# Performance work log

Hardware: AMD Instinct MI355X
Metric: run time of the kernel (lower is better)

Reference implementation:

```python
import jax, jax.numpy as jnp
import numpy as np

EPS = 1e-12  # matches torch F.normalize default eps

def setup_inputs() -> dict:
    key = jax.random.key(0)
    k1, k2 = jax.random.split(key)
    query = jax.random.normal(k1, (8, 2048, 512), dtype=jnp.float32)
    support = jax.random.normal(k2, (8, 4096, 512), dtype=jnp.float32)
    return {"query": query, "support": support}

def _l2_normalize(x):
    # torch.nn.functional.normalize(x, dim=-1): x / max(||x||, eps)
    n = jnp.sqrt(jnp.sum(x * x, axis=-1, keepdims=True))
    return x / jnp.maximum(n, EPS)

def reference(query, support):
    # cosine distance: 1 - q_hat @ s_hat^T  -> [B, Nq, Ns]
    qn = _l2_normalize(query)
    sn = _l2_normalize(support)
    dist = 1.0 - jnp.einsum('bqd,bsd->bqs', qn, sn)
    min_d = jnp.min(dist, axis=2)        # [B, Nq]
    return jnp.mean(min_d, axis=1)       # [B]
```

## Files before the change

### kernel.cpp

```cpp
#include <hip/hip_runtime.h>
#include <hip/hip_bf16.h>

typedef __attribute__((ext_vector_type(8))) short short8;
typedef __attribute__((ext_vector_type(4))) float f32x4;
typedef __attribute__((ext_vector_type(16))) float f32x16;
typedef __attribute__((ext_vector_type(8))) int int8v;

#define D   512
#define NQ  2048
#define NS  4096
#define NB  8
#define BM  128
#define BN  128
#define BK  32

typedef const __attribute__((address_space(1))) unsigned int gas_uint;
typedef __attribute__((address_space(3))) unsigned int las_uint;

__device__ __forceinline__ short f2bf(float f) {
  unsigned u = __builtin_bit_cast(unsigned, f);
  unsigned r = u + 0x7fffu + ((u >> 16) & 1u);
  return (short)(r >> 16);
}

__device__ __forceinline__ short8 pack8(float4 a, float4 b, float r) {
  short8 o;
  o[0] = f2bf(a.x * r); o[1] = f2bf(a.y * r); o[2] = f2bf(a.z * r); o[3] = f2bf(a.w * r);
  o[4] = f2bf(b.x * r); o[5] = f2bf(b.y * r); o[6] = f2bf(b.z * r); o[7] = f2bf(b.w * r);
  return o;
}

__global__ void normcvt8_kernel(const float* __restrict__ q, const float* __restrict__ s,
                                unsigned char* __restrict__ qn, unsigned char* __restrict__ sn,
                                unsigned* __restrict__ maxenc) {
  if (blockIdx.x < 64) maxenc[(blockIdx.x << 8) | threadIdx.x] = 0;
  int wave = blockIdx.x * 4 + (threadIdx.x >> 6);
  int lane = threadIdx.x & 63;
  const int NQR = NB * NQ;
  const float4* src; unsigned char* dst;
  if (wave < NQR) { src = (const float4*)(q + (size_t)wave * D); dst = qn + (size_t)wave * D; }
  else {
    size_t w = wave - NQR;
    src = (const float4*)(s + w * D); dst = sn + w * D;
  }
  float4 a = src[lane * 2];
  float4 b = src[lane * 2 + 1];
  float ss = a.x*a.x + a.y*a.y + a.z*a.z + a.w*a.w
           + b.x*b.x + b.y*b.y + b.z*b.z + b.w*b.w;
  #pragma unroll
  for (int m = 32; m >= 1; m >>= 1) ss += __shfl_xor(ss, m, 64);
  float r = 1.0f / fmaxf(sqrtf(ss), 1e-12f);
  int w0 = __builtin_amdgcn_cvt_pk_fp8_f32(a.x * r, a.y * r, 0, false);
  w0     = __builtin_amdgcn_cvt_pk_fp8_f32(a.z * r, a.w * r, w0, true);
  int w1 = __builtin_amdgcn_cvt_pk_fp8_f32(b.x * r, b.y * r, 0, false);
  w1     = __builtin_amdgcn_cvt_pk_fp8_f32(b.z * r, b.w * r, w1, true);
  *(int2*)(dst + lane * 8) = make_int2(w0, w1);
}

__global__ __launch_bounds__(512, 4) void cosmax5_kernel(
    const unsigned char* __restrict__ Qn, const unsigned char* __restrict__ Sn,
    unsigned int* __restrict__ maxenc)
{
  __shared__ __align__(16) unsigned char As[BM * 128];
  __shared__ __align__(16) unsigned char Bs[BN * 128];
  __shared__ float maxbuf[BM][2];

  const int b  = blockIdx.z;
  const int mt = blockIdx.y;
  const int nt = blockIdx.x;
  const int tid  = threadIdx.x;
  const int wave = tid >> 6;
  const int lane = tid & 63;

  const int srow   = lane >> 3;
  const int schunk = (lane & 7) ^ srow;
  const unsigned char* gA = Qn + ((size_t)b * NQ + (size_t)mt * BM + wave * 16 + srow) * D + schunk * 16;
  const unsigned char* gB = Sn + ((size_t)b * NS + (size_t)nt * BN + wave * 16 + srow) * D + schunk * 16;
  unsigned char* lA = As + wave * 2048;
  unsigned char* lB = Bs + wave * 2048;

  const int l31 = lane & 31, kc = lane >> 5;
  const int mstrip = wave & 3, nhalf = wave >> 2;
  const int rA = mstrip * 32 + l31;
  const int rB = nhalf * 64 + l31;
  const int swA = (rA * 128) ^ ((rA & 7) * 16) ^ (kc * 32);
  const int swB = (rB * 128) ^ ((rB & 7) * 16) ^ (kc * 32);

  f32x16 acc[2];
  #pragma unroll
  for (int j = 0; j < 2; ++j)
    #pragma unroll
    for (int r = 0; r < 16; ++r) acc[j][r] = 0.f;

  for (int kt = 0; kt < 4; ++kt) {
    const int ko = kt * 128;
    #pragma unroll
    for (int t = 0; t < 2; ++t) {
      __builtin_amdgcn_global_load_lds((gas_uint*)(gA + t * 8 * D + ko), (las_uint*)(lA + t * 1024), 16, 0, 0);
      __builtin_amdgcn_global_load_lds((gas_uint*)(gB + t * 8 * D + ko), (las_uint*)(lB + t * 1024), 16, 0, 0);
    }
    __syncthreads();

    #pragma unroll
    for (int s = 0; s < 2; ++s) {
      const int c0 = s * 64, c1 = s * 64 + 16;
      int8v a, b0, b1;
      ((int4*)&a)[0]  = *(const int4*)&As[swA ^ c0];
      ((int4*)&a)[1]  = *(const int4*)&As[swA ^ c1];
      ((int4*)&b0)[0] = *(const int4*)&Bs[swB ^ c0];
      ((int4*)&b0)[1] = *(const int4*)&Bs[swB ^ c1];
      acc[0] = __builtin_amdgcn_mfma_scale_f32_32x32x64_f8f6f4(
          a, b0, acc[0], 0, 0, 0, 0x7f7f7f7f, 0, 0x7f7f7f7f);
      ((int4*)&b1)[0] = *(const int4*)&Bs[(swB ^ c0) + 4096];
      ((int4*)&b1)[1] = *(const int4*)&Bs[(swB ^ c1) + 4096];
      acc[1] = __builtin_amdgcn_mfma_scale_f32_32x32x64_f8f6f4(
          a, b1, acc[1], 0, 0, 0, 0x7f7f7f7f, 0, 0x7f7f7f7f);
    }
    __syncthreads();
  }

  #pragma unroll
  for (int r = 0; r < 16; ++r) {
    float v = fmaxf(acc[0][r], acc[1][r]);
    v = fmaxf(v, __shfl_xor(v, 1, 64));
    v = fmaxf(v, __shfl_xor(v, 2, 64));
    v = fmaxf(v, __shfl_xor(v, 4, 64));
    v = fmaxf(v, __shfl_xor(v, 8, 64));
    v = fmaxf(v, __shfl_xor(v, 16, 64));
    if (l31 == 0) {
      int row = mstrip * 32 + (r & 3) + 8 * (r >> 2) + 4 * kc;
      maxbuf[row][nhalf] = v;
    }
  }
  __syncthreads();

  if (tid < BM) {
    float v = fmaxf(maxbuf[tid][0], maxbuf[tid][1]);
    unsigned e = __builtin_bit_cast(unsigned, v);
    e = ((int)e >= 0) ? (e | 0x80000000u) : ~e;
    atomicMax(&maxenc[(size_t)b * NQ + mt * BM + tid], e);
  }
}

__global__ void finalize_kernel(const unsigned* __restrict__ maxenc,
                                float* __restrict__ out) {
  int b = blockIdx.x;
  int tid = threadIdx.x;
  float sum = 0.f;
  for (int i = tid; i < NQ; i += 256) {
    unsigned e = maxenc[(size_t)b * NQ + i];
    unsigned u = (e & 0x80000000u) ? (e & 0x7fffffffu) : ~e;
    float v = __builtin_bit_cast(float, u);
    sum += 1.0f - v;
  }
  #pragma unroll
  for (int m = 32; m >= 1; m >>= 1) sum += __shfl_xor(sum, m, 64);
  __shared__ float part[4];
  if ((tid & 63) == 0) part[tid >> 6] = sum;
  __syncthreads();
  if (tid == 0) out[b] = (part[0] + part[1] + part[2] + part[3]) * (1.0f / (float)NQ);
}

__global__ void norms_kernel(const float* __restrict__ q, const float* __restrict__ s,
                             float* __restrict__ rq, float* __restrict__ rs) {
  int wave = blockIdx.x * 4 + (threadIdx.x >> 6);
  int lane = threadIdx.x & 63;
  const int NQR = NB * NQ, NSR = NB * NS;
  if (wave >= NQR + NSR) return;
  const float4* r4; float* outp;
  if (wave < NQR) { r4 = (const float4*)(q + (size_t)wave * D); outp = rq + wave; }
  else           { r4 = (const float4*)(s + (size_t)(wave - NQR) * D); outp = rs + (wave - NQR); }
  float4 a = r4[lane];
  float4 b = r4[lane + 64];
  float ss = a.x*a.x + a.y*a.y + a.z*a.z + a.w*a.w
           + b.x*b.x + b.y*b.y + b.z*b.z + b.w*b.w;
  #pragma unroll
  for (int m = 32; m >= 1; m >>= 1) ss += __shfl_xor(ss, m, 64);
  if (lane == 0) *outp = 1.0f / fmaxf(sqrtf(ss), 1e-12f);
}

__global__ __launch_bounds__(256, 3) void cosmax_kernel(
    const float* __restrict__ Q, const float* __restrict__ S,
    const float* __restrict__ rq, const float* __restrict__ rs,
    unsigned int* __restrict__ maxenc)
{
  __shared__ short As[BM * BK];
  __shared__ short Bs[BN * BK];
  __shared__ float maxbuf[BM][2];

  const int b  = blockIdx.z, mt = blockIdx.y, nt = blockIdx.x;
  const float* Qb  = Q + ((size_t)b * NQ + mt * BM) * D;
  const float* Sb  = S + ((size_t)b * NS + nt * BN) * D;
  const float* rqb = rq + (size_t)b * NQ + mt * BM;
  const float* rsb = rs + (size_t)b * NS + nt * BN;

  const int tid  = threadIdx.x;
  const int srow = tid >> 2;
  const int kseg = (tid & 3) * 8;
  const float rq0 = rqb[srow], rq1 = rqb[srow + 64];
  const float rs0 = rsb[srow], rs1 = rsb[srow + 64];
  const int wave = tid >> 6, lane = tid & 63;
  const int wm = (wave & 1) * 64, wn = (wave >> 1) * 64;
  const int lm = lane & 15, lk = (lane >> 4) * 8;

  f32x4 acc[4][4];
  #pragma unroll
  for (int i = 0; i < 4; ++i)
    #pragma unroll
    for (int j = 0; j < 4; ++j) acc[i][j] = (f32x4){0.f, 0.f, 0.f, 0.f};

  const float* qrow0 = Qb + (size_t)srow * D + kseg;
  const float* qrow1 = qrow0 + (size_t)64 * D;
  const float* srow0 = Sb + (size_t)srow * D + kseg;
  const float* srow1 = srow0 + (size_t)64 * D;

  float4 qa, qb2, qc, qd, sa, sb2, sc, sd;
  #define LOADK(k0)                                                    \
    qa  = *(const float4*)(qrow0 + (k0));  qb2 = *(const float4*)(qrow0 + (k0) + 4); \
    qc  = *(const float4*)(qrow1 + (k0));  qd  = *(const float4*)(qrow1 + (k0) + 4); \
    sa  = *(const float4*)(srow0 + (k0));  sb2 = *(const float4*)(srow0 + (k0) + 4); \
    sc  = *(const float4*)(srow1 + (k0));  sd  = *(const float4*)(srow1 + (k0) + 4);
  LOADK(0);
  #pragma unroll 4
  for (int kt = 0; kt < D / BK; ++kt) {
    *(short8*)&As[srow        * BK + kseg] = pack8(qa, qb2, rq0);
    *(short8*)&As[(srow + 64) * BK + kseg] = pack8(qc, qd,  rq1);
    *(short8*)&Bs[srow        * BK + kseg] = pack8(sa, sb2, rs0);
    *(short8*)&Bs[(srow + 64) * BK + kseg] = pack8(sc, sd,  rs1);
    __syncthreads();
    if (kt < D / BK - 1) { LOADK((kt + 1) * BK); }
    short8 af[4], bf[4];
    #pragma unroll
    for (int i = 0; i < 4; ++i) af[i] = *(short8*)&As[(wm + i * 16 + lm) * BK + lk];
    #pragma unroll
    for (int j = 0; j < 4; ++j) bf[j] = *(short8*)&Bs[(wn + j * 16 + lm) * BK + lk];
    #pragma unroll
    for (int i = 0; i < 4; ++i)
      #pragma unroll
      for (int j = 0; j < 4; ++j)
        acc[i][j] = __builtin_amdgcn_mfma_f32_16x16x32_bf16(af[i], bf[j], acc[i][j], 0, 0, 0);
    __syncthreads();
  }
  #undef LOADK

  #pragma unroll
  for (int i = 0; i < 4; ++i) {
    #pragma unroll
    for (int r = 0; r < 4; ++r) {
      float v = fmaxf(fmaxf(acc[i][0][r], acc[i][1][r]),
                      fmaxf(acc[i][2][r], acc[i][3][r]));
      v = fmaxf(v, __shfl_xor(v, 1, 64));
      v = fmaxf(v, __shfl_xor(v, 2, 64));
      v = fmaxf(v, __shfl_xor(v, 4, 64));
      v = fmaxf(v, __shfl_xor(v, 8, 64));
      if ((lane & 15) == 0) {
        int row = wm + i * 16 + (lane >> 4) * 4 + r;
        maxbuf[row][wave >> 1] = v;
      }
    }
  }
  __syncthreads();
  if (tid < BM) {
    float v = fmaxf(maxbuf[tid][0], maxbuf[tid][1]);
    unsigned e = __builtin_bit_cast(unsigned, v);
    e = ((int)e >= 0) ? (e | 0x80000000u) : ~e;
    atomicMax(&maxenc[(size_t)b * NQ + mt * BM + tid], e);
  }
}

extern "C" void kernel_launch(void* const* d_in, const int* in_sizes, int n_in,
                              void* d_out, int out_size, void* d_ws, size_t ws_size,
                              hipStream_t stream) {
  const float* q = (const float*)d_in[0];
  const float* s = (const float*)d_in[1];
  float* out = (float*)d_out;

  unsigned* maxenc = (unsigned*)d_ws;
  const size_t QOFF = 65536;
  const size_t SOFF = QOFF + (size_t)NB * NQ * D;
  const size_t NEED = SOFF + (size_t)NB * NS * D;

  dim3 grid(NS / BN, NQ / BM, NB);

  if (ws_size >= NEED) {
    unsigned char* qn = (unsigned char*)d_ws + QOFF;
    unsigned char* sn = (unsigned char*)d_ws + SOFF;
    normcvt8_kernel<<<NB * (NQ + NS) / 4, 256, 0, stream>>>(q, s, qn, sn, maxenc);
    cosmax5_kernel<<<grid, 512, 0, stream>>>(qn, sn, maxenc);
    finalize_kernel<<<NB, 256, 0, stream>>>(maxenc, out);
  } else {
    float* rq = (float*)((char*)d_ws + 65536);
    float* rs = (float*)((char*)d_ws + 131072);
    hipMemsetAsync(maxenc, 0, (size_t)NB * NQ * sizeof(unsigned), stream);
    norms_kernel<<<NB * (NQ + NS) / 4, 256, 0, stream>>>(q, s, rq, rs);
    cosmax_kernel<<<grid, 256, 0, stream>>>(q, s, rq, rs, maxenc);
    finalize_kernel<<<NB, 256, 0, stream>>>(maxenc, out);
  }
}
```

Measured before the change: 189.6 us.

## Double-buffer LDS tiles to overlap global loads with FP8 MFMA compute

Splits the A and B shared-memory tiles into two buffers. The first K-slice is prefetched before the loop, and each iteration issues the async global-to-LDS load for the next slice before running MFMAs on the current one, with one barrier per iteration instead of two. The goal is to hide global load latency behind matrix-core work. The cost is double the LDS per block, which can cut how many blocks fit on a CU, and the K loop is only four iterations long, so there is little to overlap.

```diff
diff --git a/kernel.cpp b/kernel.cpp
--- a/kernel.cpp
+++ b/kernel.cpp
@@ -57,12 +57,12 @@
   *(int2*)(dst + lane * 8) = make_int2(w0, w1);
 }
 
-__global__ __launch_bounds__(512, 4) void cosmax5_kernel(
+__global__ __launch_bounds__(512, 4) void cosmax6_kernel(
     const unsigned char* __restrict__ Qn, const unsigned char* __restrict__ Sn,
     unsigned int* __restrict__ maxenc)
 {
-  __shared__ __align__(16) unsigned char As[BM * 128];
-  __shared__ __align__(16) unsigned char Bs[BN * 128];
+  __shared__ __align__(16) unsigned char As[2][BM * 128];
+  __shared__ __align__(16) unsigned char Bs[2][BN * 128];
   __shared__ float maxbuf[BM][2];
 
   const int b  = blockIdx.z;
@@ -76,8 +76,7 @@
   const int schunk = (lane & 7) ^ srow;
   const unsigned char* gA = Qn + ((size_t)b * NQ + (size_t)mt * BM + wave * 16 + srow) * D + schunk * 16;
   const unsigned char* gB = Sn + ((size_t)b * NS + (size_t)nt * BN + wave * 16 + srow) * D + schunk * 16;
-  unsigned char* lA = As + wave * 2048;
-  unsigned char* lB = Bs + wave * 2048;
+  const int lso = wave * 2048;
 
   const int l31 = lane & 31, kc = lane >> 5;
   const int mstrip = wave & 3, nhalf = wave >> 2;
@@ -92,31 +91,43 @@
     #pragma unroll
     for (int r = 0; r < 16; ++r) acc[j][r] = 0.f;
 
+  #pragma unroll
+  for (int t = 0; t < 2; ++t) {
+    __builtin_amdgcn_global_load_lds((gas_uint*)(gA + t * 8 * D), (las_uint*)(&As[0][lso + t * 1024]), 16, 0, 0);
+    __builtin_amdgcn_global_load_lds((gas_uint*)(gB + t * 8 * D), (las_uint*)(&Bs[0][lso + t * 1024]), 16, 0, 0);
+  }
+
+  #pragma unroll
   for (int kt = 0; kt < 4; ++kt) {
-    const int ko = kt * 128;
-    #pragma unroll
-    for (int t = 0; t < 2; ++t) {
-      __builtin_amdgcn_global_load_lds((gas_uint*)(gA + t * 8 * D + ko), (las_uint*)(lA + t * 1024), 16, 0, 0);
-      __builtin_amdgcn_global_load_lds((gas_uint*)(gB + t * 8 * D + ko), (las_uint*)(lB + t * 1024), 16, 0, 0);
+    const int cur = kt & 1, nxt = cur ^ 1;
+    __syncthreads();
+
+    if (kt < 3) {
+      const int ko = (kt + 1) * 128;
+      #pragma unroll
+      for (int t = 0; t < 2; ++t) {
+        __builtin_amdgcn_global_load_lds((gas_uint*)(gA + t * 8 * D + ko), (las_uint*)(&As[nxt][lso + t * 1024]), 16, 0, 0);
+        __builtin_amdgcn_global_load_lds((gas_uint*)(gB + t * 8 * D + ko), (las_uint*)(&Bs[nxt][lso + t * 1024]), 16, 0, 0);
+      }
     }
-    __syncthreads();
-
+
+    const unsigned char* Ab = As[cur];
+    const unsigned char* Bb = Bs[cur];
     #pragma unroll
     for (int s = 0; s < 2; ++s) {
       const int c0 = s * 64, c1 = s * 64 + 16;
       int8v a, b0, b1;
-      ((int4*)&a)[0]  = *(const int4*)&As[swA ^ c0];
-      ((int4*)&a)[1]  = *(const int4*)&As[swA ^ c1];
-      ((int4*)&b0)[0] = *(const int4*)&Bs[swB ^ c0];
-      ((int4*)&b0)[1] = *(const int4*)&Bs[swB ^ c1];
+      ((int4*)&a)[0]  = *(const int4*)&Ab[swA ^ c0];
+      ((int4*)&a)[1]  = *(const int4*)&Ab[swA ^ c1];
+      ((int4*)&b0)[0] = *(const int4*)&Bb[swB ^ c0];
+      ((int4*)&b0)[1] = *(const int4*)&Bb[swB ^ c1];
       acc[0] = __builtin_amdgcn_mfma_scale_f32_32x32x64_f8f6f4(
           a, b0, acc[0], 0, 0, 0, 0x7f7f7f7f, 0, 0x7f7f7f7f);
-      ((int4*)&b1)[0] = *(const int4*)&Bs[(swB ^ c0) + 4096];
-      ((int4*)&b1)[1] = *(const int4*)&Bs[(swB ^ c1) + 4096];
+      ((int4*)&b1)[0] = *(const int4*)&Bb[(swB ^ c0) + 4096];
+      ((int4*)&b1)[1] = *(const int4*)&Bb[(swB ^ c1) + 4096];
       acc[1] = __builtin_amdgcn_mfma_scale_f32_32x32x64_f8f6f4(
           a, b1, acc[1], 0, 0, 0, 0x7f7f7f7f, 0, 0x7f7f7f7f);
     }
-    __syncthreads();
   }
 
   #pragma unroll
@@ -286,7 +297,7 @@
     unsigned char* qn = (unsigned char*)d_ws + QOFF;
     unsigned char* sn = (unsigned char*)d_ws + SOFF;
     normcvt8_kernel<<<NB * (NQ + NS) / 4, 256, 0, stream>>>(q, s, qn, sn, maxenc);
-    cosmax5_kernel<<<grid, 512, 0, stream>>>(qn, sn, maxenc);
+    cosmax6_kernel<<<grid, 512, 0, stream>>>(qn, sn, maxenc);
     finalize_kernel<<<NB, 256, 0, stream>>>(maxenc, out);
   } else {
     float* rq = (float*)((char*)d_ws + 65536);
```

Result: slower. 198.5 us (+4.7%).

## Keep query tile in registers and stream support tiles through triple-buffered LDS

Applied to the files above, without the earlier changes.

Replaces the per-tile cosine-max kernel with one where each 256-thread block loads a 64-row query tile once, keeps its fp8 fragments in registers, and streams 2048 support rows through a three-slot LDS ring using async global-to-LDS loads and manual waitcnt/barriers. Running row maxima are kept in registers across support tiles, which greatly reduces the number of atomicMax calls and query reloads. The intent is to overlap global loads with MFMA work and to remove the repeated A-tile traffic. In exchange the grid shrinks to 2x32x8 blocks (512 total), which may leave CUs underused, and the hand-written wait counts have to match the number of loads in flight.

```diff
diff --git a/kernel.cpp b/kernel.cpp
--- a/kernel.cpp
+++ b/kernel.cpp
@@ -16,6 +16,10 @@
 
 typedef const __attribute__((address_space(1))) unsigned int gas_uint;
 typedef __attribute__((address_space(3))) unsigned int las_uint;
+
+#define WAIT_VM4   0x0F74
+#define WAIT_VM0   0x0F70
+#define WAIT_LGKM0 0xC07F
 
 __device__ __forceinline__ short f2bf(float f) {
   unsigned u = __builtin_bit_cast(unsigned, f);
@@ -57,88 +61,152 @@
   *(int2*)(dst + lane * 8) = make_int2(w0, w1);
 }
 
-__global__ __launch_bounds__(512, 4) void cosmax5_kernel(
+__global__ __launch_bounds__(256) void cosmax7_kernel(
     const unsigned char* __restrict__ Qn, const unsigned char* __restrict__ Sn,
     unsigned int* __restrict__ maxenc)
 {
-  __shared__ __align__(16) unsigned char As[BM * 128];
-  __shared__ __align__(16) unsigned char Bs[BN * 128];
-  __shared__ float maxbuf[BM][2];
-
-  const int b  = blockIdx.z;
-  const int mt = blockIdx.y;
-  const int nt = blockIdx.x;
+  __shared__ __align__(16) unsigned char sbuf[49152];
+  __shared__ float maxbuf[64][2];
+
+  const int b   = blockIdx.z;
+  const int mt  = blockIdx.y;
+  const int nsp = blockIdx.x;
   const int tid  = threadIdx.x;
   const int wave = tid >> 6;
   const int lane = tid & 63;
-
-  const int srow   = lane >> 3;
-  const int schunk = (lane & 7) ^ srow;
-  const unsigned char* gA = Qn + ((size_t)b * NQ + (size_t)mt * BM + wave * 16 + srow) * D + schunk * 16;
-  const unsigned char* gB = Sn + ((size_t)b * NS + (size_t)nt * BN + wave * 16 + srow) * D + schunk * 16;
-  unsigned char* lA = As + wave * 2048;
-  unsigned char* lB = Bs + wave * 2048;
-
   const int l31 = lane & 31, kc = lane >> 5;
-  const int mstrip = wave & 3, nhalf = wave >> 2;
-  const int rA = mstrip * 32 + l31;
-  const int rB = nhalf * 64 + l31;
-  const int swA = (rA * 128) ^ ((rA & 7) * 16) ^ (kc * 32);
-  const int swB = (rB * 128) ^ ((rB & 7) * 16) ^ (kc * 32);
-
-  f32x16 acc[2];
-  #pragma unroll
-  for (int j = 0; j < 2; ++j)
-    #pragma unroll
-    for (int r = 0; r < 16; ++r) acc[j][r] = 0.f;
-
-  for (int kt = 0; kt < 4; ++kt) {
-    const int ko = kt * 128;
-    #pragma unroll
-    for (int t = 0; t < 2; ++t) {
-      __builtin_amdgcn_global_load_lds((gas_uint*)(gA + t * 8 * D + ko), (las_uint*)(lA + t * 1024), 16, 0, 0);
-      __builtin_amdgcn_global_load_lds((gas_uint*)(gB + t * 8 * D + ko), (las_uint*)(lB + t * 1024), 16, 0, 0);
+  const int mstrip = wave & 1, nhalf = wave >> 1;
+
+  {
+    const unsigned char* Qbase = Qn + ((size_t)b * NQ + (size_t)mt * 64) * D;
+    const int baserow = wave * 2 + (lane >> 5);
+    #pragma unroll
+    for (int p = 0; p < 8; ++p) {
+      int row = p * 8 + baserow;
+      int g   = (lane & 31) ^ (row & 31);
+      __builtin_amdgcn_global_load_lds(
+          (gas_uint*)(Qbase + (size_t)row * D + g * 16),
+          (las_uint*)(sbuf + 16384 + p * 4096 + wave * 1024), 16, 0, 0);
     }
-    __syncthreads();
-
-    #pragma unroll
-    for (int s = 0; s < 2; ++s) {
-      const int c0 = s * 64, c1 = s * 64 + 16;
-      int8v a, b0, b1;
-      ((int4*)&a)[0]  = *(const int4*)&As[swA ^ c0];
-      ((int4*)&a)[1]  = *(const int4*)&As[swA ^ c1];
-      ((int4*)&b0)[0] = *(const int4*)&Bs[swB ^ c0];
-      ((int4*)&b0)[1] = *(const int4*)&Bs[swB ^ c1];
-      acc[0] = __builtin_amdgcn_mfma_scale_f32_32x32x64_f8f6f4(
-          a, b0, acc[0], 0, 0, 0, 0x7f7f7f7f, 0, 0x7f7f7f7f);
-      ((int4*)&b1)[0] = *(const int4*)&Bs[(swB ^ c0) + 4096];
-      ((int4*)&b1)[1] = *(const int4*)&Bs[(swB ^ c1) + 4096];
-      acc[1] = __builtin_amdgcn_mfma_scale_f32_32x32x64_f8f6f4(
-          a, b1, acc[1], 0, 0, 0, 0x7f7f7f7f, 0, 0x7f7f7f7f);
+  }
+  __syncthreads();
+
+  const int srow8 = lane >> 3;
+  const int sch   = (lane & 7) ^ srow8;
+  const unsigned char* gS = Sn +
+      ((size_t)b * NS + (size_t)nsp * 2048 + wave * 32 + srow8) * D + sch * 16;
+
+  auto issue = [&](size_t goff, int ldsoff) {
+    #pragma unroll
+    for (int t = 0; t < 4; ++t)
+      __builtin_amdgcn_global_load_lds((gas_uint*)(gS + goff + (size_t)t * 4096),
+          (las_uint*)(sbuf + ldsoff + wave * 4096 + t * 1024), 16, 0, 0);
+  };
+
+  issue(0, 0);
+
+  const int arow = mstrip * 32 + l31;
+  int8v a[8];
+  #pragma unroll
+  for (int kk = 0; kk < 8; ++kk) {
+    int c0 = (4 * kk + 2 * kc) ^ l31;
+    ((int4*)&a[kk])[0] = *(const int4*)&sbuf[16384 + arow * 512 + c0 * 16];
+    ((int4*)&a[kk])[1] = *(const int4*)&sbuf[16384 + arow * 512 + (c0 ^ 1) * 16];
+  }
+  __builtin_amdgcn_s_waitcnt(WAIT_LGKM0);
+  asm volatile("" ::: "memory");
+  __builtin_amdgcn_s_barrier();
+  asm volatile("" ::: "memory");
+  issue(128, 16384);
+
+  const int brow0 = (nhalf * 64 + l31) * 128;
+  const int brow1 = brow0 + 4096;
+  const int cxor  = ((kc * 2) ^ (l31 & 7)) * 16;
+
+  f32x16 acc0, acc1;
+  float rmax[16];
+  #pragma unroll
+  for (int r = 0; r < 16; ++r) rmax[r] = -2.0f;
+
+  int rd = 0, wr = 32768;
+
+  auto computeK = [&](int kt, int rdo) {
+    const unsigned char* Bb = sbuf + rdo;
+    #pragma unroll
+    for (int ss = 0; ss < 2; ++ss) {
+      const int cb = cxor ^ (ss * 64);
+      int8v b0, b1;
+      ((int4*)&b0)[0] = *(const int4*)&Bb[brow0 + cb];
+      ((int4*)&b0)[1] = *(const int4*)&Bb[brow0 + (cb ^ 16)];
+      ((int4*)&b1)[0] = *(const int4*)&Bb[brow1 + cb];
+      ((int4*)&b1)[1] = *(const int4*)&Bb[brow1 + (cb ^ 16)];
+      acc0 = __builtin_amdgcn_mfma_scale_f32_32x32x64_f8f6f4(
+          a[kt * 2 + ss], b0, acc0, 0, 0, 0, 0x7f7f7f7f, 0, 0x7f7f7f7f);
+      acc1 = __builtin_amdgcn_mfma_scale_f32_32x32x64_f8f6f4(
+          a[kt * 2 + ss], b1, acc1, 0, 0, 0, 0x7f7f7f7f, 0, 0x7f7f7f7f);
     }
-    __syncthreads();
-  }
+  };
+
+  #define ROT(x) x = (x == 32768) ? 0 : x + 16384
+
+  for (int nt2 = 0; nt2 < 16; ++nt2) {
+    const size_t ntb = (size_t)nt2 << 16;
+
+    __builtin_amdgcn_s_waitcnt(WAIT_VM4);
+    asm volatile("" ::: "memory");
+    __builtin_amdgcn_s_barrier();
+    asm volatile("" ::: "memory");
+    issue(ntb + 256, wr); ROT(wr);
+    #pragma unroll
+    for (int r = 0; r < 16; ++r) { acc0[r] = 0.f; acc1[r] = 0.f; }
+    computeK(0, rd); ROT(rd);
+
+    __builtin_amdgcn_s_waitcnt(WAIT_VM4);
+    asm volatile("" ::: "memory");
+    __builtin_amdgcn_s_barrier();
+    asm volatile("" ::: "memory");
+    issue(ntb + 384, wr); ROT(wr);
+    computeK(1, rd); ROT(rd);
+
+    __builtin_amdgcn_s_waitcnt(WAIT_VM4);
+    asm volatile("" ::: "memory");
+    __builtin_amdgcn_s_barrier();
+    asm volatile("" ::: "memory");
+    if (nt2 < 15) { issue(ntb + 65536, wr); ROT(wr); }
+    computeK(2, rd); ROT(rd);
+
+    if (nt2 < 15) __builtin_amdgcn_s_waitcnt(WAIT_VM4);
+    else          __builtin_amdgcn_s_waitcnt(WAIT_VM0);
+    asm volatile("" ::: "memory");
+    __builtin_amdgcn_s_barrier();
+    asm volatile("" ::: "memory");
+    if (nt2 < 15) { issue(ntb + 65536 + 128, wr); ROT(wr); }
+    computeK(3, rd); ROT(rd);
+
+    #pragma unroll
+    for (int r = 0; r < 16; ++r)
+      rmax[r] = fmaxf(rmax[r], fmaxf(acc0[r], acc1[r]));
+  }
+  #undef ROT
 
   #pragma unroll
   for (int r = 0; r < 16; ++r) {
-    float v = fmaxf(acc[0][r], acc[1][r]);
+    float v = rmax[r];
     v = fmaxf(v, __shfl_xor(v, 1, 64));
     v = fmaxf(v, __shfl_xor(v, 2, 64));
     v = fmaxf(v, __shfl_xor(v, 4, 64));
     v = fmaxf(v, __shfl_xor(v, 8, 64));
     v = fmaxf(v, __shfl_xor(v, 16, 64));
-    if (l31 == 0) {
-      int row = mstrip * 32 + (r & 3) + 8 * (r >> 2) + 4 * kc;
-      maxbuf[row][nhalf] = v;
-    }
+    if (l31 == 0)
+      maxbuf[mstrip * 32 + (r & 3) + 8 * (r >> 2) + 4 * kc][nhalf] = v;
   }
   __syncthreads();
 
-  if (tid < BM) {
+  if (tid < 64) {
     float v = fmaxf(maxbuf[tid][0], maxbuf[tid][1]);
     unsigned e = __builtin_bit_cast(unsigned, v);
     e = ((int)e >= 0) ? (e | 0x80000000u) : ~e;
-    atomicMax(&maxenc[(size_t)b * NQ + mt * BM + tid], e);
+    atomicMax(&maxenc[(size_t)b * NQ + (size_t)mt * 64 + tid], e);
   }
 }
 
@@ -280,19 +348,19 @@
   const size_t SOFF = QOFF + (size_t)NB * NQ * D;
   const size_t NEED = SOFF + (size_t)NB * NS * D;
 
-  dim3 grid(NS / BN, NQ / BM, NB);
-
   if (ws_size >= NEED) {
     unsigned char* qn = (unsigned char*)d_ws + QOFF;
     unsigned char* sn = (unsigned char*)d_ws + SOFF;
     normcvt8_kernel<<<NB * (NQ + NS) / 4, 256, 0, stream>>>(q, s, qn, sn, maxenc);
-    cosmax5_kernel<<<grid, 512, 0, stream>>>(qn, sn, maxenc);
+    dim3 grid7(2, NQ / 64, NB);
+    cosmax7_kernel<<<grid7, 256, 0, stream>>>(qn, sn, maxenc);
     finalize_kernel<<<NB, 256, 0, stream>>>(maxenc, out);
   } else {
     float* rq = (float*)((char*)d_ws + 65536);
     float* rs = (float*)((char*)d_ws + 131072);
     hipMemsetAsync(maxenc, 0, (size_t)NB * NQ * sizeof(unsigned), stream);
     norms_kernel<<<NB * (NQ + NS) / 4, 256, 0, stream>>>(q, s, rq, rs);
+    dim3 grid(NS / BN, NQ / BM, NB);
     cosmax_kernel<<<grid, 256, 0, stream>>>(q, s, rq, rs, maxenc);
     finalize_kernel<<<NB, 256, 0, stream>>>(maxenc, out);
   }
```

Result: faster. 166.7 us (-12.0%).
